# Kernel optimization log

Measured on AMD Instinct MI355X. Metric: run time of the kernel, lower is better.

## Reference

```python
import jax, jax.numpy as jnp
import numpy as np

NUM_EXPERTS = 64
TOP_K = 2

def setup_inputs() -> dict:
    key = jax.random.key(0)
    k1, k2, k3, k4 = jax.random.split(key, 4)
    B, N, C, E = 4, 4096, 2048, NUM_EXPERTS
    x = jax.random.normal(k1, (B, N, C), dtype=jnp.float32)
    routing_context = jax.random.normal(k2, (B, C), dtype=jnp.float32)
    # Linear(C, E, bias=False) and Linear(C, C, bias=False), torch layout (out, in)
    gate_w = jax.random.normal(k3, (E, C), dtype=jnp.float32) * (1.0 / np.sqrt(C))
    ctx_w = jax.random.normal(k4, (C, C), dtype=jnp.float32) * (1.0 / np.sqrt(C))
    return {"x": x, "routing_context": routing_context, "gate_w": gate_w, "ctx_w": ctx_w}

def reference(x, routing_context, gate_w, ctx_w):
    B, N, C = x.shape
    T = B * N
    E = gate_w.shape[0]
    # context_proj(routing_context): (B,C) @ (C,C)^T -> broadcast over N
    ctx = routing_context @ ctx_w.T                      # (B, C)
    x_routing = (x + ctx[:, None, :]).reshape(T, C)      # (T, C)
    logits = x_routing @ gate_w.T                        # (T, E)
    top_vals, top_idx = jax.lax.top_k(logits, TOP_K)     # (T, K) each
    top_weights = jax.nn.softmax(top_vals, axis=-1)      # (T, K)
    probs = jax.nn.softmax(logits, axis=-1)              # (T, E)
    importance = probs.sum(axis=0) / T                   # (E,)
    # load: fraction of tokens that pick each expert in their top-k
    load = jnp.zeros((E,), dtype=probs.dtype).at[top_idx.reshape(-1)].add(1.0) / T
    aux_loss = E * (importance * load).sum()
    return top_idx, top_weights, aux_loss
```

## Files before the change

kernel.cpp:

```cpp
#include <hip/hip_runtime.h>
#include <math.h>

#define T_TOKENS 16384
#define C_DIM    2048
#define N_SEQ    4096
#define E_EXP    64
#define GN       131072
#define FBLK     512

typedef __attribute__((ext_vector_type(8))) short  short8;
typedef __attribute__((ext_vector_type(4))) float  floatx4;

__device__ __forceinline__ void splitv(float v, ushort& h, ushort& m, ushort& l) {
    unsigned u = __float_as_uint(v);
    h = (ushort)(u >> 16);
    float f1 = v - __uint_as_float(u & 0xffff0000u);
    unsigned u1 = __float_as_uint(f1);
    m = (ushort)(u1 >> 16);
    float f2 = f1 - __uint_as_float(u1 & 0xffff0000u);
    l = (ushort)(__float_as_uint(f2) >> 16);
}

__device__ __forceinline__ void splitpack8(const float4& a, const float4& b,
                                           short8& h, short8& m, short8& l) {
    ushort hh, mm, ll;
    splitv(a.x, hh, mm, ll); h[0] = hh; m[0] = mm; l[0] = ll;
    splitv(a.y, hh, mm, ll); h[1] = hh; m[1] = mm; l[1] = ll;
    splitv(a.z, hh, mm, ll); h[2] = hh; m[2] = mm; l[2] = ll;
    splitv(a.w, hh, mm, ll); h[3] = hh; m[3] = mm; l[3] = ll;
    splitv(b.x, hh, mm, ll); h[4] = hh; m[4] = mm; l[4] = ll;
    splitv(b.y, hh, mm, ll); h[5] = hh; m[5] = mm; l[5] = ll;
    splitv(b.z, hh, mm, ll); h[6] = hh; m[6] = mm; l[6] = ll;
    splitv(b.w, hh, mm, ll); h[7] = hh; m[7] = mm; l[7] = ll;
}

__device__ __forceinline__ void split3rne(float v, ushort& h, ushort& m, ushort& l) {
    unsigned u = __float_as_uint(v);
    unsigned r = (u + 0x7fffu + ((u >> 16) & 1u)) >> 16;
    h = (ushort)r;
    float e1 = v - __uint_as_float(r << 16);
    u = __float_as_uint(e1);
    r = (u + 0x7fffu + ((u >> 16) & 1u)) >> 16;
    m = (ushort)r;
    float e2 = e1 - __uint_as_float(r << 16);
    l = (ushort)(__float_as_uint(e2) >> 16);
}

__device__ __forceinline__ void ctx_body(
    int j, int lane, const float* __restrict__ rc,
    const float* __restrict__ ctx_w, float* __restrict__ ctx_out)
{
    const float4* wr = (const float4*)(ctx_w + (size_t)j * C_DIM);
    const float4* r0 = (const float4*)(rc);
    const float4* r1 = (const float4*)(rc + C_DIM);
    const float4* r2 = (const float4*)(rc + 2 * C_DIM);
    const float4* r3 = (const float4*)(rc + 3 * C_DIM);

    float s0 = 0.f, s1 = 0.f, s2 = 0.f, s3 = 0.f;
#pragma unroll
    for (int it = 0; it < 8; ++it) {
        float4 a  = wr[it * 64 + lane];
        float4 c0 = r0[it * 64 + lane];
        float4 c1 = r1[it * 64 + lane];
        float4 c2 = r2[it * 64 + lane];
        float4 c3 = r3[it * 64 + lane];
        s0 += a.x * c0.x + a.y * c0.y + a.z * c0.z + a.w * c0.w;
        s1 += a.x * c1.x + a.y * c1.y + a.z * c1.z + a.w * c1.w;
        s2 += a.x * c2.x + a.y * c2.y + a.z * c2.z + a.w * c2.w;
        s3 += a.x * c3.x + a.y * c3.y + a.z * c3.z + a.w * c3.w;
    }
#pragma unroll
    for (int off = 32; off; off >>= 1) {
        s0 += __shfl_xor(s0, off, 64);
        s1 += __shfl_xor(s1, off, 64);
        s2 += __shfl_xor(s2, off, 64);
        s3 += __shfl_xor(s3, off, 64);
    }
    if (lane == 0) {
        ctx_out[j]             = s0;
        ctx_out[C_DIM + j]     = s1;
        ctx_out[2 * C_DIM + j] = s2;
        ctx_out[3 * C_DIM + j] = s3;
    }
}

__global__ __launch_bounds__(256) void pre_kernel(
    const float* __restrict__ rc, const float* __restrict__ ctx_w,
    const float* __restrict__ gw, float* __restrict__ ctx_out,
    ushort* __restrict__ gsp)
{
    if (gsp != nullptr) {
        const int idx  = blockIdx.x * 256 + threadIdx.x;
        const int j    = idx & 7;
        const int e    = (idx >> 3) & 63;
        const int koct = idx >> 9;
        float g = gw[(size_t)e * C_DIM + koct * 8 + j];
        ushort h, m, l;
        split3rne(g, h, m, l);
        gsp[idx]          = h;
        gsp[GN + idx]     = m;
        gsp[2 * GN + idx] = l;
    }
    const int lane = threadIdx.x & 63;
    const int j    = blockIdx.x * 4 + (threadIdx.x >> 6);
    ctx_body(j, lane, rc, ctx_w, ctx_out);
}

__global__ __launch_bounds__(256) void cl_kernel(
    const float* __restrict__ gw, const float* __restrict__ ctx,
    float* __restrict__ cl)
{
    const int lane = threadIdx.x & 63;
    const int pk   = blockIdx.x * 4 + (threadIdx.x >> 6);
    const int b    = pk >> 6;
    const int e    = pk & 63;
    const float4* wr = (const float4*)(gw + (size_t)e * C_DIM);
    const float4* cr = (const float4*)(ctx + (size_t)b * C_DIM);
    float s = 0.f;
#pragma unroll
    for (int it = 0; it < 8; ++it) {
        float4 a = wr[it * 64 + lane];
        float4 c = cr[it * 64 + lane];
        s += a.x * c.x + a.y * c.y + a.z * c.z + a.w * c.w;
    }
#pragma unroll
    for (int off = 32; off; off >>= 1) s += __shfl_xor(s, off, 64);
    if (lane == 0) cl[pk] = s;
}

__global__ __launch_bounds__(128, 1) void fused_kernel(
    const float* __restrict__ x, const ushort* __restrict__ gsp,
    const float* __restrict__ cl, float* __restrict__ out,
    float* __restrict__ bp)
{
    __shared__ float red[2][128];

    const int tid  = threadIdx.x;
    const int wv   = tid >> 6;
    const int lane = tid & 63;
    const int l15  = lane & 15;
    const int quad = lane >> 4;
    const int t0   = blockIdx.x * 32;
    const int b    = t0 >> 12;

    floatx4 acc[4];
#pragma unroll
    for (int nt = 0; nt < 4; ++nt) acc[nt] = (floatx4){0.f, 0.f, 0.f, 0.f};

    const float* xr = x + (size_t)(t0 + wv * 16 + l15) * C_DIM + quad * 8;

    float4 a00 = *(const float4*)(xr);
    float4 a01 = *(const float4*)(xr + 4);
    float4 n00 = *(const float4*)(xr + 32);
    float4 n01 = *(const float4*)(xr + 36);

#pragma unroll 2
    for (int ks = 0; ks < 64; ++ks) {
        const int fk = (ks + 2 < 64) ? ks + 2 : 0;
        float4 f00 = *(const float4*)(xr + fk * 32);
        float4 f01 = *(const float4*)(xr + fk * 32 + 4);

        const ushort* bks = gsp + ((size_t)(ks * 4 + quad) * 64 + l15) * 8;
        short8 bh[4], bm[4], bl[4];
#pragma unroll
        for (int nt = 0; nt < 4; ++nt) {
            const ushort* bp_ = bks + (size_t)(16 * nt) * 8;
            bh[nt] = *(const short8*)(bp_);
            bm[nt] = *(const short8*)(bp_ + GN);
            bl[nt] = *(const short8*)(bp_ + 2 * (size_t)GN);
        }

        short8 ah, am, al;
        splitpack8(a00, a01, ah, am, al);

#pragma unroll
        for (int nt = 0; nt < 4; ++nt) {
            acc[nt] = __builtin_amdgcn_mfma_f32_16x16x32_bf16(ah, bh[nt], acc[nt], 0, 0, 0);
            acc[nt] = __builtin_amdgcn_mfma_f32_16x16x32_bf16(ah, bm[nt], acc[nt], 0, 0, 0);
            acc[nt] = __builtin_amdgcn_mfma_f32_16x16x32_bf16(am, bh[nt], acc[nt], 0, 0, 0);
            acc[nt] = __builtin_amdgcn_mfma_f32_16x16x32_bf16(ah, bl[nt], acc[nt], 0, 0, 0);
            acc[nt] = __builtin_amdgcn_mfma_f32_16x16x32_bf16(al, bh[nt], acc[nt], 0, 0, 0);
            acc[nt] = __builtin_amdgcn_mfma_f32_16x16x32_bf16(am, bm[nt], acc[nt], 0, 0, 0);
        }

        a00 = n00; a01 = n01; n00 = f00; n01 = f01;
    }

    float clv[4];
#pragma unroll
    for (int nt = 0; nt < 4; ++nt) clv[nt] = cl[b * 64 + 16 * nt + l15];

    float imp4[4] = {0.f, 0.f, 0.f, 0.f};
    float cnt4[4] = {0.f, 0.f, 0.f, 0.f};

#pragma unroll
    for (int r = 0; r < 4; ++r) {
        const int t = t0 + wv * 16 + quad * 4 + r;
        float v[4], p[4];
#pragma unroll
        for (int nt = 0; nt < 4; ++nt) {
            v[nt] = acc[nt][r] + clv[nt];
            p[nt] = expf(v[nt]);
        }
        float s = (p[0] + p[1]) + (p[2] + p[3]);

        float v1 = v[0];      int i1 = l15;
        float v2 = -INFINITY; int i2 = 0x7fffffff;
#pragma unroll
        for (int k = 1; k < 4; ++k) {
            const int e = 16 * k + l15;
            if (v[k] > v1) { v2 = v1; i2 = i1; v1 = v[k]; i1 = e; }
            else if (v[k] > v2 || (v[k] == v2 && e < i2)) { v2 = v[k]; i2 = e; }
        }

#pragma unroll
        for (int off = 8; off; off >>= 1) {
            float ov1 = __shfl_xor(v1, off, 64);
            int   oi1 = __shfl_xor(i1, off, 64);
            float ov2 = __shfl_xor(v2, off, 64);
            int   oi2 = __shfl_xor(i2, off, 64);
            s += __shfl_xor(s, off, 64);
            const bool aw = (ov1 < v1) || (ov1 == v1 && i1 < oi1);
            const float lv = aw ? ov1 : v1;  const int li = aw ? oi1 : i1;
            const float wv2 = aw ? v2 : ov2; const int wi = aw ? i2 : oi2;
            if (!aw) { v1 = ov1; i1 = oi1; }
            const bool sw = (wv2 < lv) || (wv2 == lv && li < wi);
            v2 = sw ? lv : wv2; i2 = sw ? li : wi;
        }

#pragma unroll
        for (int nt = 0; nt < 4; ++nt) {
            const int e = 16 * nt + l15;
            imp4[nt] += p[nt] / s;
            cnt4[nt] += ((e == i1) ? 1.f : 0.f) + ((e == i2) ? 1.f : 0.f);
        }

        if (l15 == 0) {
            const float e2 = expf(v2 - v1);
            out[2 * t]     = (float)i1;
            out[2 * t + 1] = (float)i2;
            out[2 * T_TOKENS + 2 * t]     = 1.f / (1.f + e2);
            out[2 * T_TOKENS + 2 * t + 1] = e2 / (1.f + e2);
        }
    }

#pragma unroll
    for (int nt = 0; nt < 4; ++nt) {
        imp4[nt] += __shfl_xor(imp4[nt], 16, 64);
        imp4[nt] += __shfl_xor(imp4[nt], 32, 64);
        cnt4[nt] += __shfl_xor(cnt4[nt], 16, 64);
        cnt4[nt] += __shfl_xor(cnt4[nt], 32, 64);
    }
    if (quad == 0) {
#pragma unroll
        for (int nt = 0; nt < 4; ++nt) {
            red[wv][16 * nt + l15]      = imp4[nt];
            red[wv][64 + 16 * nt + l15] = cnt4[nt];
        }
    }
    __syncthreads();
    if (tid < 128)
        bp[(size_t)blockIdx.x * 128 + tid] = red[0][tid] + red[1][tid];
}

__global__ __launch_bounds__(1024) void aux_kernel(
    const float* __restrict__ bp, int nb, float* __restrict__ out_aux)
{
    __shared__ float4 red[32][32];
    const int tid = threadIdx.x;
    const int c4  = tid & 31;
    const int grp = tid >> 5;

    const float4* bp4 = (const float4*)bp;
    float4 s = make_float4(0.f, 0.f, 0.f, 0.f);
    for (int r = grp; r < nb; r += 32) {
        float4 v = bp4[(size_t)r * 32 + c4];
        s.x += v.x; s.y += v.y; s.z += v.z; s.w += v.w;
    }
    red[grp][c4] = s;
    __syncthreads();

    if (tid < 32) {
        float4 t = make_float4(0.f, 0.f, 0.f, 0.f);
#pragma unroll
        for (int g = 0; g < 32; ++g) {
            float4 v = red[g][tid];
            t.x += v.x; t.y += v.y; t.z += v.z; t.w += v.w;
        }
        red[0][tid] = t;
    }
    __syncthreads();

    if (tid < 16) {
        float4 a = red[0][tid];
        float4 b = red[0][tid + 16];
        float v = a.x * b.x + a.y * b.y + a.z * b.z + a.w * b.w;
#pragma unroll
        for (int off = 8; off; off >>= 1) v += __shfl_xor(v, off, 64);
        if (tid == 0)
            out_aux[0] = (float)E_EXP * v / ((float)T_TOKENS * (float)T_TOKENS);
    }
}

#define TM    64
#define FKC   64
#define FLSTR 68
__global__ __launch_bounds__(256) void router_fused_kernel(
    const float* __restrict__ x, const float* __restrict__ gate_w,
    const float* __restrict__ ctx, float* __restrict__ out,
    float* __restrict__ bp)
{
    __shared__ float xs[TM][FLSTR];
    __shared__ float gs[E_EXP][FLSTR];
    __shared__ float ls[TM][FLSTR];
    __shared__ float red[4][128];

    const int tid = threadIdx.x;
    const int eg  = tid & 15;
    const int tg  = tid >> 4;
    const int t0  = blockIdx.x * TM;
    const int b   = t0 / N_SEQ;
    const int sr  = tid >> 4;
    const int scg = tid & 15;
    const float* ctx_row = ctx + (size_t)b * C_DIM;

    float4 acc[4][4];
#pragma unroll
    for (int i = 0; i < 4; ++i)
#pragma unroll
        for (int j = 0; j < 4; ++j) acc[i][j] = make_float4(0.f, 0.f, 0.f, 0.f);

    float4 px[4], pg[4], pc;
    auto prefetch = [&](int kc) {
        const int c0 = kc * FKC + scg * 4;
        pc = *(const float4*)(ctx_row + c0);
#pragma unroll
        for (int i = 0; i < 4; ++i) {
            px[i] = *(const float4*)(x + (size_t)(t0 + sr + 16 * i) * C_DIM + c0);
            pg[i] = *(const float4*)(gate_w + (size_t)(sr + 16 * i) * C_DIM + c0);
        }
    };

    prefetch(0);
    const int NCHUNK = C_DIM / FKC;
    for (int kc = 0; kc < NCHUNK; ++kc) {
        __syncthreads();
#pragma unroll
        for (int i = 0; i < 4; ++i) {
            float4 v = px[i];
            v.x += pc.x; v.y += pc.y; v.z += pc.z; v.w += pc.w;
            *(float4*)&xs[sr + 16 * i][scg * 4] = v;
            *(float4*)&gs[sr + 16 * i][scg * 4] = pg[i];
        }
        __syncthreads();
        if (kc + 1 < NCHUNK) prefetch(kc + 1);
#pragma unroll
        for (int cc = 0; cc < FKC; cc += 4) {
            float4 xv[4], gv[4];
#pragma unroll
            for (int i = 0; i < 4; ++i) xv[i] = *(const float4*)&xs[tg + 16 * i][cc];
#pragma unroll
            for (int j = 0; j < 4; ++j) gv[j] = *(const float4*)&gs[eg + 16 * j][cc];
#pragma unroll
            for (int i = 0; i < 4; ++i)
#pragma unroll
                for (int j = 0; j < 4; ++j) {
                    acc[i][j].x = fmaf(xv[i].x, gv[j].x, acc[i][j].x);
                    acc[i][j].y = fmaf(xv[i].y, gv[j].y, acc[i][j].y);
                    acc[i][j].z = fmaf(xv[i].z, gv[j].z, acc[i][j].z);
                    acc[i][j].w = fmaf(xv[i].w, gv[j].w, acc[i][j].w);
                }
        }
    }

    __syncthreads();
#pragma unroll
    for (int i = 0; i < 4; ++i)
#pragma unroll
        for (int j = 0; j < 4; ++j)
            ls[tg + 16 * i][eg + 16 * j] =
                (acc[i][j].x + acc[i][j].y) + (acc[i][j].z + acc[i][j].w);
    __syncthreads();

    const int wv   = tid >> 6;
    const int lane = tid & 63;
    float imp_acc = 0.f, cnt_acc = 0.f;

    for (int tt = 0; tt < 16; ++tt) {
        const int tokL = wv * 16 + tt;
        const float v = ls[tokL][lane];
        const float p = expf(v);
        float v1 = v;  int i1 = lane;
        float v2 = -INFINITY; int i2 = 0x7fffffff;
        float s = p;
#pragma unroll
        for (int off = 32; off; off >>= 1) {
            float ov1 = __shfl_xor(v1, off, 64);
            int   oi1 = __shfl_xor(i1, off, 64);
            float ov2 = __shfl_xor(v2, off, 64);
            int   oi2 = __shfl_xor(i2, off, 64);
            s += __shfl_xor(s, off, 64);
            const bool aw = (ov1 < v1) || (ov1 == v1 && i1 < oi1);
            const float lv = aw ? ov1 : v1;  const int li = aw ? oi1 : i1;
            const float wv2 = aw ? v2 : ov2; const int wi = aw ? i2 : oi2;
            if (!aw) { v1 = ov1; i1 = oi1; }
            const bool sw = (wv2 < lv) || (wv2 == lv && li < wi);
            v2 = sw ? lv : wv2; i2 = sw ? li : wi;
        }
        imp_acc += p / s;
        if (lane == i1 || lane == i2) cnt_acc += 1.f;
        if (lane == 0) {
            const int t = t0 + tokL;
            const float e2 = expf(v2 - v1);
            out[2 * t]     = (float)i1;
            out[2 * t + 1] = (float)i2;
            out[2 * T_TOKENS + 2 * t]     = 1.f / (1.f + e2);
            out[2 * T_TOKENS + 2 * t + 1] = e2 / (1.f + e2);
        }
    }

    red[wv][lane]      = imp_acc;
    red[wv][64 + lane] = cnt_acc;
    __syncthreads();
    if (tid < 128) {
        float s = red[0][tid] + red[1][tid] + red[2][tid] + red[3][tid];
        bp[(size_t)blockIdx.x * 128 + tid] = s;
    }
}

extern "C" void kernel_launch(void* const* d_in, const int* in_sizes, int n_in,
                              void* d_out, int out_size, void* d_ws, size_t ws_size,
                              hipStream_t stream)
{
    (void)in_sizes; (void)n_in; (void)out_size;
    const float* x      = (const float*)d_in[0];
    const float* rc     = (const float*)d_in[1];
    const float* gate_w = (const float*)d_in[2];
    const float* ctx_w  = (const float*)d_in[3];
    float* out = (float*)d_out;

    float*  ctx = (float*)d_ws;
    float*  cl  = ctx + 8192;
    float*  bp  = cl + 256;
    ushort* gsp = (ushort*)(bp + (size_t)FBLK * 128);

    const size_t need =
        (8192 + 256 + (size_t)FBLK * 128) * sizeof(float)
        + (size_t)3 * GN * sizeof(ushort);

    if (ws_size >= need) {
        pre_kernel<<<512, 256, 0, stream>>>(rc, ctx_w, gate_w, ctx, gsp);
        cl_kernel<<<64, 256, 0, stream>>>(gate_w, ctx, cl);
        fused_kernel<<<FBLK, 128, 0, stream>>>(x, gsp, cl, out, bp);
        aux_kernel<<<1, 1024, 0, stream>>>(bp, FBLK, out + 2 * 2 * T_TOKENS);
    } else {
        pre_kernel<<<512, 256, 0, stream>>>(rc, ctx_w, gate_w, ctx, nullptr);
        router_fused_kernel<<<256, 256, 0, stream>>>(x, gate_w, ctx, out, bp);
        aux_kernel<<<1, 1024, 0, stream>>>(bp, 256, out + 2 * 2 * T_TOKENS);
    }
}
```

Baseline: 254.0 us.

## Stage gate-weight split tiles through double-buffered LDS with swizzle, deepen x prefetch

Each k-step's three bf16 split planes of the gate weights are now loaded cooperatively by both waves into a double-buffered shared-memory tile (with an XOR swizzle to avoid bank conflicts). Previously each wave fetched its B fragments directly from global memory. The x prefetch distance is also raised from 2 to 4 k-steps. The aim is to halve redundant global/L2 traffic for the weights and hide more load latency. In exchange it adds one __syncthreads per iteration, extra registers and LDS use.

```diff
diff --git a/kernel.cpp b/kernel.cpp
--- a/kernel.cpp
+++ b/kernel.cpp
@@ -133,7 +133,8 @@
     const float* __restrict__ cl, float* __restrict__ out,
     float* __restrict__ bp)
 {
-    __shared__ float red[2][128];
+    __shared__ ushort Bs[2][3][2048];
+    __shared__ float  red[2][128];
 
     const int tid  = threadIdx.x;
     const int wv   = tid >> 6;
@@ -149,41 +150,71 @@
 
     const float* xr = x + (size_t)(t0 + wv * 16 + l15) * C_DIM + quad * 8;
 
-    float4 a00 = *(const float4*)(xr);
-    float4 a01 = *(const float4*)(xr + 4);
-    float4 n00 = *(const float4*)(xr + 32);
-    float4 n01 = *(const float4*)(xr + 36);
+    const int sl0 = tid * 8;
+    const int sl1 = (tid + 128) * 8;
+    const int sw0 = sl0 ^ (((sl0 >> 9) & 3) << 3);
+    const int sw1 = sl1 ^ (((sl1 >> 9) & 3) << 3);
+
+    int roff[4];
+#pragma unroll
+    for (int nt = 0; nt < 4; ++nt)
+        roff[nt] = quad * 512 + (((16 * nt + l15) ^ quad) << 3);
+
+    short8 s00 = *(const short8*)(gsp + 0 * (size_t)GN + sw0);
+    short8 s01 = *(const short8*)(gsp + 0 * (size_t)GN + sw1);
+    short8 s10 = *(const short8*)(gsp + 1 * (size_t)GN + sw0);
+    short8 s11 = *(const short8*)(gsp + 1 * (size_t)GN + sw1);
+    short8 s20 = *(const short8*)(gsp + 2 * (size_t)GN + sw0);
+    short8 s21 = *(const short8*)(gsp + 2 * (size_t)GN + sw1);
+    float4 pa0 = *(const float4*)(xr);       float4 pa1 = *(const float4*)(xr + 4);
+    float4 pb0 = *(const float4*)(xr + 32);  float4 pb1 = *(const float4*)(xr + 36);
+    float4 pc0 = *(const float4*)(xr + 64);  float4 pc1 = *(const float4*)(xr + 68);
+    float4 pd0 = *(const float4*)(xr + 96);  float4 pd1 = *(const float4*)(xr + 100);
 
 #pragma unroll 2
     for (int ks = 0; ks < 64; ++ks) {
-        const int fk = (ks + 2 < 64) ? ks + 2 : 0;
-        float4 f00 = *(const float4*)(xr + fk * 32);
-        float4 f01 = *(const float4*)(xr + fk * 32 + 4);
-
-        const ushort* bks = gsp + ((size_t)(ks * 4 + quad) * 64 + l15) * 8;
-        short8 bh[4], bm[4], bl[4];
+        ushort* bw = &Bs[ks & 1][0][0];
+        *(short8*)(bw + 0 * 2048 + sl0) = s00;
+        *(short8*)(bw + 0 * 2048 + sl1) = s01;
+        *(short8*)(bw + 1 * 2048 + sl0) = s10;
+        *(short8*)(bw + 1 * 2048 + sl1) = s11;
+        *(short8*)(bw + 2 * 2048 + sl0) = s20;
+        *(short8*)(bw + 2 * 2048 + sl1) = s21;
+
+        const int nk = (ks + 1 < 64) ? ks + 1 : 0;
+        const size_t nb_ = (size_t)nk * 2048;
+        s00 = *(const short8*)(gsp + 0 * (size_t)GN + nb_ + sw0);
+        s01 = *(const short8*)(gsp + 0 * (size_t)GN + nb_ + sw1);
+        s10 = *(const short8*)(gsp + 1 * (size_t)GN + nb_ + sw0);
+        s11 = *(const short8*)(gsp + 1 * (size_t)GN + nb_ + sw1);
+        s20 = *(const short8*)(gsp + 2 * (size_t)GN + nb_ + sw0);
+        s21 = *(const short8*)(gsp + 2 * (size_t)GN + nb_ + sw1);
+
+        const int fk = (ks + 4 < 64) ? ks + 4 : 0;
+        float4 f0 = *(const float4*)(xr + fk * 32);
+        float4 f1 = *(const float4*)(xr + fk * 32 + 4);
+
+        short8 ah, am, al;
+        splitpack8(pa0, pa1, ah, am, al);
+
+        __syncthreads();
+
+        const ushort* br = &Bs[ks & 1][0][0];
 #pragma unroll
         for (int nt = 0; nt < 4; ++nt) {
-            const ushort* bp_ = bks + (size_t)(16 * nt) * 8;
-            bh[nt] = *(const short8*)(bp_);
-            bm[nt] = *(const short8*)(bp_ + GN);
-            bl[nt] = *(const short8*)(bp_ + 2 * (size_t)GN);
-        }
-
-        short8 ah, am, al;
-        splitpack8(a00, a01, ah, am, al);
-
-#pragma unroll
-        for (int nt = 0; nt < 4; ++nt) {
-            acc[nt] = __builtin_amdgcn_mfma_f32_16x16x32_bf16(ah, bh[nt], acc[nt], 0, 0, 0);
-            acc[nt] = __builtin_amdgcn_mfma_f32_16x16x32_bf16(ah, bm[nt], acc[nt], 0, 0, 0);
-            acc[nt] = __builtin_amdgcn_mfma_f32_16x16x32_bf16(am, bh[nt], acc[nt], 0, 0, 0);
-            acc[nt] = __builtin_amdgcn_mfma_f32_16x16x32_bf16(ah, bl[nt], acc[nt], 0, 0, 0);
-            acc[nt] = __builtin_amdgcn_mfma_f32_16x16x32_bf16(al, bh[nt], acc[nt], 0, 0, 0);
-            acc[nt] = __builtin_amdgcn_mfma_f32_16x16x32_bf16(am, bm[nt], acc[nt], 0, 0, 0);
-        }
-
-        a00 = n00; a01 = n01; n00 = f00; n01 = f01;
+            short8 bh = *(const short8*)(br + 0 * 2048 + roff[nt]);
+            short8 bm = *(const short8*)(br + 1 * 2048 + roff[nt]);
+            short8 bl = *(const short8*)(br + 2 * 2048 + roff[nt]);
+            acc[nt] = __builtin_amdgcn_mfma_f32_16x16x32_bf16(ah, bh, acc[nt], 0, 0, 0);
+            acc[nt] = __builtin_amdgcn_mfma_f32_16x16x32_bf16(ah, bm, acc[nt], 0, 0, 0);
+            acc[nt] = __builtin_amdgcn_mfma_f32_16x16x32_bf16(am, bh, acc[nt], 0, 0, 0);
+            acc[nt] = __builtin_amdgcn_mfma_f32_16x16x32_bf16(ah, bl, acc[nt], 0, 0, 0);
+            acc[nt] = __builtin_amdgcn_mfma_f32_16x16x32_bf16(al, bh, acc[nt], 0, 0, 0);
+            acc[nt] = __builtin_amdgcn_mfma_f32_16x16x32_bf16(am, bm, acc[nt], 0, 0, 0);
+        }
+
+        pa0 = pb0; pa1 = pb1; pb0 = pc0; pb1 = pc1;
+        pc0 = pd0; pc1 = pd1; pd0 = f0;  pd1 = f1;
     }
 
     float clv[4];
```

Result: faster. 242.2 us (-4.6%).
